# Optimization experiments

Measured on AMD Instinct MI355X. Metric: run time of the kernel, lower is better.

The kernel has to match this reference:

```python
import jax, jax.numpy as jnp
import numpy as np

N_ATOMS = 500_000
N_BONDS = 600_000
N_MOL = 25_000
DEG_COUNTS = [100_000, 175_000, 150_000, 75_000]  # degrees 1..4, sum = N_ATOMS
ATOM_F, BOND_F = 62, 6
HID, FP = 100, 512


def setup_inputs() -> dict:
    key = jax.random.key(0)
    ks = jax.random.split(key, 32)
    inp = {}
    inp['atom_features'] = jax.random.normal(ks[0], (N_ATOMS, ATOM_F), dtype=jnp.float32)
    inp['bond_features'] = jax.random.normal(ks[1], (N_BONDS, BOND_F), dtype=jnp.float32)
    for i, (name_a, name_b, n) in enumerate(zip(['an1','an2','an3','an4'], ['bn1','bn2','bn3','bn4'], DEG_COUNTS)):
        d = i + 1
        inp[name_a] = jax.random.randint(ks[2 + 2*i], (n, d), 0, N_ATOMS, dtype=jnp.int32)
        inp[name_b] = jax.random.randint(ks[3 + 2*i], (n, d), 0, N_BONDS, dtype=jnp.int32)
    inp['mol_ids'] = jnp.repeat(jnp.arange(N_MOL, dtype=jnp.int32), N_ATOMS // N_MOL)
    dims = [(ATOM_F, HID), (HID, HID), (HID, FP)]
    for li, (din, dout) in enumerate(dims):
        inp[f'Wself{li}'] = jax.random.normal(ks[12 + li], (din, dout), dtype=jnp.float32) * (din ** -0.5)
        inp[f'bself{li}'] = jax.random.normal(ks[15 + li], (dout,), dtype=jnp.float32) * 0.01
        inp[f'Wd{li}'] = jax.random.normal(ks[18 + li], (4, din + BOND_F, dout), dtype=jnp.float32) * ((din + BOND_F) ** -0.5)
        inp[f'bd{li}'] = jax.random.normal(ks[21 + li], (4, dout), dtype=jnp.float32) * 0.01
    return inp


def _forward(atom_features, bond_features, ans, bns, mol_ids, self_params, deg_params):
    x = atom_features
    for (Ws, bs), (Wd, bd) in zip(self_params, deg_params):
        self_logits = x @ Ws + bs                      # [N, out]
        neigh = []
        for d in range(4):                             # degrees 1..4 (structurally distinct)
            a_sum = x[ans[d]].sum(axis=1)              # [n_d, F_in]  gather + reduce over degree
            b_sum = bond_features[bns[d]].sum(axis=1)  # [n_d, BOND_F]
            h = jnp.concatenate([a_sum, b_sum], axis=1)
            neigh.append(h @ Wd[d] + bd[d])
        neighbors_logits = jnp.concatenate(neigh, axis=0)  # atoms sorted by degree
        t = neighbors_logits + self_logits
        norm = jnp.linalg.norm(t, axis=1, keepdims=True)   # F.normalize (L2, eps=1e-12)
        x = jax.nn.relu(t / jnp.maximum(norm, 1e-12))
    return jax.ops.segment_sum(x, mol_ids, num_segments=N_MOL)  # sum_and_stack


def reference(atom_features, bond_features, an1, an2, an3, an4, bn1, bn2, bn3, bn4,
              mol_ids, Wself0, bself0, Wself1, bself1, Wself2, bself2,
              Wd0, bd0, Wd1, bd1, Wd2, bd2):
    ans = (an1, an2, an3, an4)
    bns = (bn1, bn2, bn3, bn4)
    self_params = ((Wself0, bself0), (Wself1, bself1), (Wself2, bself2))
    deg_params = ((Wd0, bd0), (Wd1, bd1), (Wd2, bd2))
    return _forward(atom_features, bond_features, ans, bns, mol_ids, self_params, deg_params)
```

## Files before the change

kernel.cpp:

```cpp
#include <hip/hip_runtime.h>


#define XS 100

typedef __attribute__((ext_vector_type(8))) short short8;
typedef __attribute__((ext_vector_type(4))) float float4v;

__device__ __forceinline__ float bf2f(unsigned u) { return __uint_as_float(u << 16); }
__device__ __forceinline__ unsigned short f2bf(float f) {
    unsigned b = __float_as_uint(f);
    return (unsigned short)((b + 0x7FFFu + ((b >> 16) & 1u)) >> 16);
}
__device__ __forceinline__ unsigned pack2(float a, float b) {
    return (unsigned)f2bf(a) | ((unsigned)f2bf(b) << 16);
}
__device__ __forceinline__ void rowseg(int r, int& deg, int& seg) {
    if (r < 100000)      { deg = 1; seg = 0;      }
    else if (r < 275000) { deg = 2; seg = 100000; }
    else if (r < 425000) { deg = 3; seg = 275000; }
    else                 { deg = 4; seg = 425000; }
}

__global__ void prep_weights(const float* __restrict__ Ws, const float* __restrict__ bs,
                             const float* __restrict__ Wd, const float* __restrict__ bd,
                             int F_IN, int F_OUT, int F_OUT_PAD, int KP, int SELF_PAD,
                             unsigned short* __restrict__ Wt, float* __restrict__ bc)
{
    int id = blockIdx.x * 256 + threadIdx.x;
    int total = 4 * F_OUT_PAD * KP;
    if (id >= total) return;
    int k  = id % KP;
    int nq = (id / KP) % F_OUT_PAD;
    int dg = id / (KP * F_OUT_PAD);
    float v = 0.f;
    if (nq < F_OUT) {
        if (k < F_IN)                                   v = Ws[(size_t)k * F_OUT + nq];
        else if (k >= SELF_PAD && k < SELF_PAD + F_IN)  v = Wd[((size_t)dg * (F_IN + 6) + (k - SELF_PAD)) * F_OUT + nq];
        else if (k >= 2 * SELF_PAD && k < 2 * SELF_PAD + 6)
            v = Wd[((size_t)dg * (F_IN + 6) + F_IN + (k - 2 * SELF_PAD)) * F_OUT + nq];
    }
    Wt[id] = f2bf(v);
    if (k == 0)
        bc[dg * F_OUT_PAD + nq] = (nq < F_OUT) ? (bs[nq] + bd[(size_t)dg * F_OUT + nq]) : 0.f;
}

template<int DEG, int SP>
__device__ __forceinline__ void g256_bf16(
    unsigned short* Hs, const unsigned short* __restrict__ x,
    const float* __restrict__ bondf,
    const int* __restrict__ an, const int* __restrict__ bn,
    int seg, int B40, int tid)
{
    const int ch  = tid & 31;
    const int rr  = tid >> 5;
    if (ch < 25) {
        int ai[5][DEG];
        #pragma unroll
        for (int p = 0; p < 5; ++p) {
            const int ri = B40 + rr + 8 * p;
            #pragma unroll
            for (int d = 0; d < DEG; ++d) ai[p][d] = an[(size_t)ri * DEG + d];
        }
        uint2 sv[5], nv[5][DEG];
        #pragma unroll
        for (int p = 0; p < 5; ++p) {
            const int atom = seg + B40 + rr + 8 * p;
            sv[p] = *(const uint2*)(x + (size_t)atom * XS + ch * 4);
            #pragma unroll
            for (int d = 0; d < DEG; ++d)
                nv[p][d] = *(const uint2*)(x + (size_t)ai[p][d] * XS + ch * 4);
        }
        #pragma unroll
        for (int p = 0; p < 5; ++p) {
            unsigned short* hrow = Hs + (rr + 8 * p) * SP;
            *(uint2*)(hrow + ch * 4) = sv[p];
            float s0 = 0.f, s1 = 0.f, s2 = 0.f, s3 = 0.f;
            #pragma unroll
            for (int d = 0; d < DEG; ++d) {
                s0 += bf2f(nv[p][d].x & 0xFFFFu); s1 += bf2f(nv[p][d].x >> 16);
                s2 += bf2f(nv[p][d].y & 0xFFFFu); s3 += bf2f(nv[p][d].y >> 16);
            }
            uint2 o; o.x = pack2(s0, s1); o.y = pack2(s2, s3);
            *(uint2*)(hrow + 104 + ch * 4) = o;
        }
    }
    if (tid < 40) {
        const int ri = B40 + tid;
        int bi[DEG];
        #pragma unroll
        for (int d = 0; d < DEG; ++d) bi[d] = bn[(size_t)ri * DEG + d];
        float2 v0[DEG], v1[DEG], v2[DEG];
        #pragma unroll
        for (int d = 0; d < DEG; ++d) {
            const float* bp = bondf + (size_t)bi[d] * 6;
            v0[d] = *(const float2*)bp;
            v1[d] = *(const float2*)(bp + 2);
            v2[d] = *(const float2*)(bp + 4);
        }
        float s0 = 0.f, s1 = 0.f, s2 = 0.f, s3 = 0.f, s4 = 0.f, s5 = 0.f;
        #pragma unroll
        for (int d = 0; d < DEG; ++d) {
            s0 += v0[d].x; s1 += v0[d].y; s2 += v1[d].x;
            s3 += v1[d].y; s4 += v2[d].x; s5 += v2[d].y;
        }
        unsigned short* hrow = Hs + tid * SP;
        uint4 w; w.x = pack2(s0, s1); w.y = pack2(s2, s3); w.z = pack2(s4, s5); w.w = 0;
        *(uint4*)(hrow + 208) = w;
        *(uint4*)(hrow + 216) = make_uint4(0, 0, 0, 0);
    }
    for (int i = tid; i < 80; i += 256) {
        unsigned short* p = Hs + (i >> 1) * SP + ((i & 1) ? 204 : 100);
        *(uint2*)p = make_uint2(0, 0);
    }
    for (int i = tid; i < 8 * 28; i += 256)
        *(uint4*)(Hs + (40 + i / 28) * SP + (i % 28) * 8) = make_uint4(0, 0, 0, 0);
}

template<int DEG, int SP>
__device__ __forceinline__ void g256_f32(
    unsigned short* Hs, const float* __restrict__ x,
    const float* __restrict__ bondf,
    const int* __restrict__ an, const int* __restrict__ bn,
    int seg, int B40, int tid)
{
    const int ch  = tid & 31;
    const int rr  = tid >> 5;
    if (ch < 31) {
        int ai[5][DEG];
        #pragma unroll
        for (int p = 0; p < 5; ++p) {
            const int ri = B40 + rr + 8 * p;
            #pragma unroll
            for (int d = 0; d < DEG; ++d) ai[p][d] = an[(size_t)ri * DEG + d];
        }
        float2 sv[5], nv[5][DEG];
        #pragma unroll
        for (int p = 0; p < 5; ++p) {
            const int atom = seg + B40 + rr + 8 * p;
            sv[p] = *(const float2*)(x + (size_t)atom * 62 + ch * 2);
            #pragma unroll
            for (int d = 0; d < DEG; ++d)
                nv[p][d] = *(const float2*)(x + (size_t)ai[p][d] * 62 + ch * 2);
        }
        #pragma unroll
        for (int p = 0; p < 5; ++p) {
            unsigned short* hrow = Hs + (rr + 8 * p) * SP;
            *(unsigned*)(hrow + ch * 2) = pack2(sv[p].x, sv[p].y);
            float s0 = 0.f, s1 = 0.f;
            #pragma unroll
            for (int d = 0; d < DEG; ++d) { s0 += nv[p][d].x; s1 += nv[p][d].y; }
            *(unsigned*)(hrow + 64 + ch * 2) = pack2(s0, s1);
        }
    }
    if (tid < 40) {
        const int ri = B40 + tid;
        int bi[DEG];
        #pragma unroll
        for (int d = 0; d < DEG; ++d) bi[d] = bn[(size_t)ri * DEG + d];
        float2 v0[DEG], v1[DEG], v2[DEG];
        #pragma unroll
        for (int d = 0; d < DEG; ++d) {
            const float* bp = bondf + (size_t)bi[d] * 6;
            v0[d] = *(const float2*)bp;
            v1[d] = *(const float2*)(bp + 2);
            v2[d] = *(const float2*)(bp + 4);
        }
        float s0 = 0.f, s1 = 0.f, s2 = 0.f, s3 = 0.f, s4 = 0.f, s5 = 0.f;
        #pragma unroll
        for (int d = 0; d < DEG; ++d) {
            s0 += v0[d].x; s1 += v0[d].y; s2 += v1[d].x;
            s3 += v1[d].y; s4 += v2[d].x; s5 += v2[d].y;
        }
        unsigned short* hrow = Hs + tid * SP;
        uint4 w; w.x = pack2(s0, s1); w.y = pack2(s2, s3); w.z = pack2(s4, s5); w.w = 0;
        *(uint4*)(hrow + 128) = w;
        *(uint4*)(hrow + 136) = make_uint4(0, 0, 0, 0);
        *(uint4*)(hrow + 144) = make_uint4(0, 0, 0, 0);
        *(uint4*)(hrow + 152) = make_uint4(0, 0, 0, 0);
    }
    for (int i = tid; i < 80; i += 256)
        *(unsigned*)(Hs + (i >> 1) * SP + ((i & 1) ? 126 : 62)) = 0;
    for (int i = tid; i < 8 * 20; i += 256)
        *(uint4*)(Hs + (40 + i / 20) * SP + (i % 20) * 8) = make_uint4(0, 0, 0, 0);
}

template<int DEG, int SP>
__device__ __forceinline__ void g512_bf16(
    unsigned short* Hs, const unsigned short* __restrict__ x,
    const float* __restrict__ bondf,
    const int* __restrict__ an, const int* __restrict__ bn,
    int seg, int B40)
{
    const int tid = threadIdx.x;
    const int ch  = tid & 31;
    const int rg  = tid >> 5;
    if (ch < 25) {
        int ai[3][DEG];
        #pragma unroll
        for (int p = 0; p < 3; ++p) {
            const int r = rg + 16 * p;
            if (r < 40) {
                const int ri = B40 + r;
                #pragma unroll
                for (int d = 0; d < DEG; ++d) ai[p][d] = an[(size_t)ri * DEG + d];
            }
        }
        uint2 sv[3], nv[3][DEG];
        #pragma unroll
        for (int p = 0; p < 3; ++p) {
            const int r = rg + 16 * p;
            if (r < 40) {
                sv[p] = *(const uint2*)(x + (size_t)(seg + B40 + r) * XS + ch * 4);
                #pragma unroll
                for (int d = 0; d < DEG; ++d)
                    nv[p][d] = *(const uint2*)(x + (size_t)ai[p][d] * XS + ch * 4);
            }
        }
        #pragma unroll
        for (int p = 0; p < 3; ++p) {
            const int r = rg + 16 * p;
            if (r < 40) {
                unsigned short* hrow = Hs + r * SP;
                *(uint2*)(hrow + ch * 4) = sv[p];
                float s0 = 0.f, s1 = 0.f, s2 = 0.f, s3 = 0.f;
                #pragma unroll
                for (int d = 0; d < DEG; ++d) {
                    s0 += bf2f(nv[p][d].x & 0xFFFFu); s1 += bf2f(nv[p][d].x >> 16);
                    s2 += bf2f(nv[p][d].y & 0xFFFFu); s3 += bf2f(nv[p][d].y >> 16);
                }
                uint2 o; o.x = pack2(s0, s1); o.y = pack2(s2, s3);
                *(uint2*)(hrow + 104 + ch * 4) = o;
            }
        }
    } else {
        const int idx = rg * 7 + (ch - 25);
        if (idx < 40) {
            const int ri = B40 + idx;
            int bi[DEG];
            #pragma unroll
            for (int d = 0; d < DEG; ++d) bi[d] = bn[(size_t)ri * DEG + d];
            float2 v0[DEG], v1[DEG], v2[DEG];
            #pragma unroll
            for (int d = 0; d < DEG; ++d) {
                const float* bp = bondf + (size_t)bi[d] * 6;
                v0[d] = *(const float2*)bp;
                v1[d] = *(const float2*)(bp + 2);
                v2[d] = *(const float2*)(bp + 4);
            }
            float s0 = 0.f, s1 = 0.f, s2 = 0.f, s3 = 0.f, s4 = 0.f, s5 = 0.f;
            #pragma unroll
            for (int d = 0; d < DEG; ++d) {
                s0 += v0[d].x; s1 += v0[d].y; s2 += v1[d].x;
                s3 += v1[d].y; s4 += v2[d].x; s5 += v2[d].y;
            }
            unsigned short* hrow = Hs + idx * SP;
            uint4 w; w.x = pack2(s0, s1); w.y = pack2(s2, s3); w.z = pack2(s4, s5); w.w = 0;
            *(uint4*)(hrow + 208) = w;
            *(uint4*)(hrow + 216) = make_uint4(0, 0, 0, 0);
        }
    }
    for (int i = tid; i < 80; i += 512) {
        unsigned short* p = Hs + (i >> 1) * SP + ((i & 1) ? 204 : 100);
        *(uint2*)p = make_uint2(0, 0);
    }
    for (int i = tid; i < 8 * 28; i += 512)
        *(uint4*)(Hs + (40 + i / 28) * SP + (i % 28) * 8) = make_uint4(0, 0, 0, 0);
}

template<int F_IN, int SELF_PAD, bool BF16IN>
__global__ __launch_bounds__(512, 4) void layer01(
    const void* __restrict__ xin,
    const float* __restrict__ bondf,
    const int* __restrict__ an1, const int* __restrict__ bn1,
    const int* __restrict__ an2, const int* __restrict__ bn2,
    const int* __restrict__ an3, const int* __restrict__ bn3,
    const int* __restrict__ an4, const int* __restrict__ bn4,
    const unsigned short* __restrict__ Wt,
    const float* __restrict__ bcomb,
    unsigned short* __restrict__ xout)
{
    constexpr int F_OUT = 100;
    constexpr int F_OUT_PAD = 112;
    constexpr int KP = (2 * SELF_PAD + 6 + 31) & ~31;
    constexpr int SP = KP + 8;

    __shared__ __align__(16) unsigned short Hs[96 * SP];
    __shared__ float ssqs[7][96];
    __shared__ __align__(16) float rn96[96];

    const int b = blockIdx.x;
    int deg, seg, pair; bool has1;
    if (b < 1250)      { deg = 1; seg = 0;      pair = b;        has1 = true; }
    else if (b < 3438) { deg = 2; seg = 100000; pair = b - 1250; has1 = (pair != 2187); }
    else if (b < 5313) { deg = 3; seg = 275000; pair = b - 3438; has1 = true; }
    else               { deg = 4; seg = 425000; pair = b - 5313; has1 = (pair != 937); }

    const int half = threadIdx.x >> 8;
    const int t    = threadIdx.x & 255;
    const int B40  = pair * 80 + half * 40;
    unsigned short* HsC = Hs + half * 48 * SP;

    if (half == 1 && !has1) {
        for (int i = t; i < 48 * SP / 8; i += 256)
            ((uint4*)HsC)[i] = make_uint4(0, 0, 0, 0);
    } else {
        if constexpr (BF16IN) {
            const unsigned short* x = (const unsigned short*)xin;
            switch (deg) {
                case 1: g256_bf16<1, SP>(HsC, x, bondf, an1, bn1, seg, B40, t); break;
                case 2: g256_bf16<2, SP>(HsC, x, bondf, an2, bn2, seg, B40, t); break;
                case 3: g256_bf16<3, SP>(HsC, x, bondf, an3, bn3, seg, B40, t); break;
                default: g256_bf16<4, SP>(HsC, x, bondf, an4, bn4, seg, B40, t); break;
            }
        } else {
            const float* x = (const float*)xin;
            switch (deg) {
                case 1: g256_f32<1, SP>(HsC, x, bondf, an1, bn1, seg, B40, t); break;
                case 2: g256_f32<2, SP>(HsC, x, bondf, an2, bn2, seg, B40, t); break;
                case 3: g256_f32<3, SP>(HsC, x, bondf, an3, bn3, seg, B40, t); break;
                default: g256_f32<4, SP>(HsC, x, bondf, an4, bn4, seg, B40, t); break;
            }
        }
    }
    __syncthreads();

    const int lane = threadIdx.x & 63;
    const int wv   = threadIdx.x >> 6;
    const int n16  = lane & 15;
    const int quad = lane >> 4;

    float4v acc[6];
    #pragma unroll
    for (int mt = 0; mt < 6; ++mt) acc[mt] = (float4v){0.f, 0.f, 0.f, 0.f};

    if (wv < 7) {
        const unsigned short* Wr =
            Wt + ((size_t)(deg - 1) * F_OUT_PAD + wv * 16 + n16) * KP;
        #pragma unroll
        for (int kk = 0; kk < KP; kk += 32) {
            short8 bb = *(const short8*)(Wr + kk + quad * 8);
            short8 a[6];
            #pragma unroll
            for (int mt = 0; mt < 6; ++mt)
                a[mt] = *(const short8*)&Hs[(mt * 16 + n16) * SP + kk + quad * 8];
            #pragma unroll
            for (int mt = 0; mt < 6; ++mt)
                acc[mt] = __builtin_amdgcn_mfma_f32_16x16x32_bf16(a[mt], bb, acc[mt], 0, 0, 0);
        }
    }

    float ssq[6][4];
    #pragma unroll
    for (int mt = 0; mt < 6; ++mt)
        #pragma unroll
        for (int r = 0; r < 4; ++r) ssq[mt][r] = 0.f;

    if (wv < 7) {
        const float bj = bcomb[(deg - 1) * F_OUT_PAD + wv * 16 + n16];
        #pragma unroll
        for (int mt = 0; mt < 6; ++mt)
            #pragma unroll
            for (int r = 0; r < 4; ++r) {
                float v = acc[mt][r] + bj;
                acc[mt][r] = v;
                ssq[mt][r] += v * v;
            }
        #pragma unroll
        for (int off = 1; off <= 8; off <<= 1)
            #pragma unroll
            for (int mt = 0; mt < 6; ++mt)
                #pragma unroll
                for (int r = 0; r < 4; ++r)
                    ssq[mt][r] += __shfl_xor(ssq[mt][r], off);
        if (n16 == 0)
            #pragma unroll
            for (int mt = 0; mt < 6; ++mt)
                #pragma unroll
                for (int r = 0; r < 4; ++r)
                    ssqs[wv][mt * 16 + quad * 4 + r] = ssq[mt][r];
    }
    __syncthreads();

    if (threadIdx.x < 96) {
        float s = 0.f;
        #pragma unroll
        for (int w = 0; w < 7; ++w) s += ssqs[w][threadIdx.x];
        rn96[threadIdx.x] = 1.0f / fmaxf(sqrtf(s), 1e-12f);
    }
    __syncthreads();

    const int col = wv * 16 + n16;
    if (wv < 7 && col < F_OUT) {
        #pragma unroll
        for (int mt = 0; mt < 6; ++mt) {
            const int chunk = mt / 3;
            if (chunk == 0 || has1) {
                float4 rv = *(const float4*)&rn96[mt * 16 + quad * 4];
                const float rn_[4] = {rv.x, rv.y, rv.z, rv.w};
                const int rowc0 = (mt % 3) * 16 + quad * 4;
                const int gbase = seg + pair * 80 + chunk * 40 + rowc0;
                #pragma unroll
                for (int r = 0; r < 4; ++r) {
                    if (rowc0 + r < 40) {
                        const float v = fmaxf(acc[mt][r] * rn_[r], 0.f);
                        xout[(size_t)(gbase + r) * XS + col] = f2bf(v);
                    }
                }
            }
        }
    }
}

__global__ __launch_bounds__(512, 4) void layer_last(
    const unsigned short* __restrict__ x,
    const float* __restrict__ bondf,
    const int* __restrict__ an1, const int* __restrict__ bn1,
    const int* __restrict__ an2, const int* __restrict__ bn2,
    const int* __restrict__ an3, const int* __restrict__ bn3,
    const int* __restrict__ an4, const int* __restrict__ bn4,
    const unsigned short* __restrict__ Wt,
    const float* __restrict__ bcomb,
    float* __restrict__ molout)
{
    constexpr int KP = 224, SP = 232, NW = 8, JMAX = 4;

    __shared__ __align__(16) unsigned short Hs[48 * SP];
    __shared__ float ssqs[NW][48];
    __shared__ __align__(16) float rn48[48];

    const int R0 = blockIdx.x * 40;
    int deg, seg; rowseg(R0, deg, seg);
    const int B40 = R0 - seg;

    switch (deg) {
        case 1: g512_bf16<1, SP>(Hs, x, bondf, an1, bn1, seg, B40); break;
        case 2: g512_bf16<2, SP>(Hs, x, bondf, an2, bn2, seg, B40); break;
        case 3: g512_bf16<3, SP>(Hs, x, bondf, an3, bn3, seg, B40); break;
        default: g512_bf16<4, SP>(Hs, x, bondf, an4, bn4, seg, B40); break;
    }
    __syncthreads();

    const int lane = threadIdx.x & 63;
    const int wv   = threadIdx.x >> 6;
    const int n16  = lane & 15;
    const int quad = lane >> 4;

    float4v acc[JMAX][3];
    #pragma unroll
    for (int j = 0; j < JMAX; ++j)
        #pragma unroll
        for (int mt = 0; mt < 3; ++mt)
            acc[j][mt] = (float4v){0.f, 0.f, 0.f, 0.f};

    const unsigned short* Wb = Wt + (size_t)(deg - 1) * 512 * KP;

    #pragma unroll
    for (int kk = 0; kk < KP; kk += 32) {
        short8 a[3];
        #pragma unroll
        for (int mt = 0; mt < 3; ++mt)
            a[mt] = *(const short8*)&Hs[(mt * 16 + n16) * SP + kk + quad * 8];
        short8 bfr[JMAX];
        #pragma unroll
        for (int j = 0; j < JMAX; ++j) {
            const int nt = wv + NW * j;
            bfr[j] = *(const short8*)(Wb + (size_t)(nt * 16 + n16) * KP + kk + quad * 8);
        }
        #pragma unroll
        for (int j = 0; j < JMAX; ++j)
            #pragma unroll
            for (int mt = 0; mt < 3; ++mt)
                acc[j][mt] = __builtin_amdgcn_mfma_f32_16x16x32_bf16(
                    a[mt], bfr[j], acc[j][mt], 0, 0, 0);
    }

    float ssq[3][4];
    #pragma unroll
    for (int mt = 0; mt < 3; ++mt)
        #pragma unroll
        for (int r = 0; r < 4; ++r) ssq[mt][r] = 0.f;

    #pragma unroll
    for (int j = 0; j < JMAX; ++j) {
        const int nt = wv + NW * j;
        const float bj = bcomb[(deg - 1) * 512 + nt * 16 + n16];
        #pragma unroll
        for (int mt = 0; mt < 3; ++mt)
            #pragma unroll
            for (int r = 0; r < 4; ++r) {
                float v = acc[j][mt][r] + bj;
                acc[j][mt][r] = v;
                ssq[mt][r] += v * v;
            }
    }
    #pragma unroll
    for (int off = 1; off <= 8; off <<= 1)
        #pragma unroll
        for (int mt = 0; mt < 3; ++mt)
            #pragma unroll
            for (int r = 0; r < 4; ++r)
                ssq[mt][r] += __shfl_xor(ssq[mt][r], off);
    if (n16 == 0)
        #pragma unroll
        for (int mt = 0; mt < 3; ++mt)
            #pragma unroll
            for (int r = 0; r < 4; ++r)
                ssqs[wv][mt * 16 + quad * 4 + r] = ssq[mt][r];
    __syncthreads();

    if (threadIdx.x < 48) {
        float s = 0.f;
        #pragma unroll
        for (int w = 0; w < NW; ++w) s += ssqs[w][threadIdx.x];
        rn48[threadIdx.x] = 1.0f / fmaxf(sqrtf(s), 1e-12f);
    }
    __syncthreads();

    float rn[3][4];
    #pragma unroll
    for (int mt = 0; mt < 3; ++mt) {
        float4 v = *(const float4*)&rn48[mt * 16 + quad * 4];
        rn[mt][0] = v.x; rn[mt][1] = v.y; rn[mt][2] = v.z; rn[mt][3] = v.w;
    }

    #pragma unroll
    for (int j = 0; j < JMAX; ++j) {
        float m0 = 0.f, m1 = 0.f;
        #pragma unroll
        for (int mt = 0; mt < 3; ++mt)
            #pragma unroll
            for (int r = 0; r < 4; ++r) {
                const int row = mt * 16 + quad * 4 + r;
                if (row < 40) {
                    const float v = fmaxf(acc[j][mt][r] * rn[mt][r], 0.f);
                    if (row < 20) m0 += v; else m1 += v;
                }
            }
        m0 += __shfl_xor(m0, 16); m0 += __shfl_xor(m0, 32);
        m1 += __shfl_xor(m1, 16); m1 += __shfl_xor(m1, 32);
        if (quad == 0) {
            const int col = (wv + NW * j) * 16 + n16;
            molout[(size_t)(2 * blockIdx.x)     * 512 + col] = m0;
            molout[(size_t)(2 * blockIdx.x + 1) * 512 + col] = m1;
        }
    }
}

extern "C" void kernel_launch(void* const* d_in, const int* in_sizes, int n_in,
                              void* d_out, int out_size, void* d_ws, size_t ws_size,
                              hipStream_t stream) {
    const bool sig_order = (in_sizes[3] != 100000);

    const float* atomf = (const float*)d_in[0];
    const float* bondf = (const float*)d_in[1];
    const int *an1, *bn1, *an2, *bn2, *an3, *bn3, *an4, *bn4;
    const float *Ws0, *bs0, *Wd0, *bd0;
    const float *Ws1, *bs1, *Wd1, *bd1;
    const float *Ws2, *bs2, *Wd2, *bd2;

    if (!sig_order) {
        an1 = (const int*)d_in[2];  bn1 = (const int*)d_in[3];
        an2 = (const int*)d_in[4];  bn2 = (const int*)d_in[5];
        an3 = (const int*)d_in[6];  bn3 = (const int*)d_in[7];
        an4 = (const int*)d_in[8];  bn4 = (const int*)d_in[9];
        Ws0 = (const float*)d_in[11]; bs0 = (const float*)d_in[12];
        Wd0 = (const float*)d_in[13]; bd0 = (const float*)d_in[14];
        Ws1 = (const float*)d_in[15]; bs1 = (const float*)d_in[16];
        Wd1 = (const float*)d_in[17]; bd1 = (const float*)d_in[18];
        Ws2 = (const float*)d_in[19]; bs2 = (const float*)d_in[20];
        Wd2 = (const float*)d_in[21]; bd2 = (const float*)d_in[22];
    } else {
        an1 = (const int*)d_in[2];  an2 = (const int*)d_in[3];
        an3 = (const int*)d_in[4];  an4 = (const int*)d_in[5];
        bn1 = (const int*)d_in[6];  bn2 = (const int*)d_in[7];
        bn3 = (const int*)d_in[8];  bn4 = (const int*)d_in[9];
        Ws0 = (const float*)d_in[11]; bs0 = (const float*)d_in[12];
        Ws1 = (const float*)d_in[13]; bs1 = (const float*)d_in[14];
        Ws2 = (const float*)d_in[15]; bs2 = (const float*)d_in[16];
        Wd0 = (const float*)d_in[17]; bd0 = (const float*)d_in[18];
        Wd1 = (const float*)d_in[19]; bd1 = (const float*)d_in[20];
        Wd2 = (const float*)d_in[21]; bd2 = (const float*)d_in[22];
    }

    char* w = (char*)d_ws;
    unsigned short* x1  = (unsigned short*)w;
    unsigned short* x2  = (unsigned short*)(w + 100000000);
    unsigned short* Wt0 = (unsigned short*)(w + 200000000);
    float*          bc0 = (float*)(w + 200143360);
    unsigned short* Wt1 = (unsigned short*)(w + 200145152);
    float*          bc1 = (float*)(w + 200345856);
    unsigned short* Wt2 = (unsigned short*)(w + 200347648);
    float*          bc2 = (float*)(w + 201265152);

    prep_weights<<<(4 * 112 * 160 + 255) / 256, 256, 0, stream>>>(
        Ws0, bs0, Wd0, bd0, 62, 100, 112, 160, 64, Wt0, bc0);
    prep_weights<<<(4 * 112 * 224 + 255) / 256, 256, 0, stream>>>(
        Ws1, bs1, Wd1, bd1, 100, 100, 112, 224, 104, Wt1, bc1);
    prep_weights<<<(4 * 512 * 224 + 255) / 256, 256, 0, stream>>>(
        Ws2, bs2, Wd2, bd2, 100, 512, 512, 224, 104, Wt2, bc2);

    layer01<62, 64, false><<<6251, 512, 0, stream>>>(
        atomf, bondf, an1, bn1, an2, bn2, an3, bn3, an4, bn4, Wt0, bc0, x1);
    layer01<100, 104, true><<<6251, 512, 0, stream>>>(
        x1, bondf, an1, bn1, an2, bn2, an3, bn3, an4, bn4, Wt1, bc1, x2);
    layer_last<<<12500, 512, 0, stream>>>(
        x2, bondf, an1, bn1, an2, bn2, an3, bn3, an4, bn4,
        Wt2, bc2, (float*)d_out);
}
```

Baseline: 778.9 us.

## Process two 40-row tiles per block in last layer to reuse weight fragments

The final 100→512 layer now handles 80 atom rows per block (two 40-row halves, each gathered by 256 threads) instead of 40. Each wave issues MFMAs over six M-tiles per loaded weight fragment, so global weight reads per row are halved and the grid shrinks from 12500 to 6251 blocks. The cost is twice the accumulator registers and a lowered occupancy hint (launch bounds 512,2), plus a doubled shared tile and padding handling for odd segment ends.

```diff
diff --git a/kernel.cpp b/kernel.cpp
--- a/kernel.cpp
+++ b/kernel.cpp
@@ -14,11 +14,12 @@
 __device__ __forceinline__ unsigned pack2(float a, float b) {
     return (unsigned)f2bf(a) | ((unsigned)f2bf(b) << 16);
 }
-__device__ __forceinline__ void rowseg(int r, int& deg, int& seg) {
-    if (r < 100000)      { deg = 1; seg = 0;      }
-    else if (r < 275000) { deg = 2; seg = 100000; }
-    else if (r < 425000) { deg = 3; seg = 275000; }
-    else                 { deg = 4; seg = 425000; }
+
+__device__ __forceinline__ void pairseg(int b, int& deg, int& seg, int& pair, bool& has1) {
+    if (b < 1250)      { deg = 1; seg = 0;      pair = b;        has1 = true; }
+    else if (b < 3438) { deg = 2; seg = 100000; pair = b - 1250; has1 = (pair != 2187); }
+    else if (b < 5313) { deg = 3; seg = 275000; pair = b - 3438; has1 = true; }
+    else               { deg = 4; seg = 425000; pair = b - 5313; has1 = (pair != 937); }
 }
 
 __global__ void prep_weights(const float* __restrict__ Ws, const float* __restrict__ bs,
@@ -184,89 +185,6 @@
         *(uint4*)(Hs + (40 + i / 20) * SP + (i % 20) * 8) = make_uint4(0, 0, 0, 0);
 }
 
-template<int DEG, int SP>
-__device__ __forceinline__ void g512_bf16(
-    unsigned short* Hs, const unsigned short* __restrict__ x,
-    const float* __restrict__ bondf,
-    const int* __restrict__ an, const int* __restrict__ bn,
-    int seg, int B40)
-{
-    const int tid = threadIdx.x;
-    const int ch  = tid & 31;
-    const int rg  = tid >> 5;
-    if (ch < 25) {
-        int ai[3][DEG];
-        #pragma unroll
-        for (int p = 0; p < 3; ++p) {
-            const int r = rg + 16 * p;
-            if (r < 40) {
-                const int ri = B40 + r;
-                #pragma unroll
-                for (int d = 0; d < DEG; ++d) ai[p][d] = an[(size_t)ri * DEG + d];
-            }
-        }
-        uint2 sv[3], nv[3][DEG];
-        #pragma unroll
-        for (int p = 0; p < 3; ++p) {
-            const int r = rg + 16 * p;
-            if (r < 40) {
-                sv[p] = *(const uint2*)(x + (size_t)(seg + B40 + r) * XS + ch * 4);
-                #pragma unroll
-                for (int d = 0; d < DEG; ++d)
-                    nv[p][d] = *(const uint2*)(x + (size_t)ai[p][d] * XS + ch * 4);
-            }
-        }
-        #pragma unroll
-        for (int p = 0; p < 3; ++p) {
-            const int r = rg + 16 * p;
-            if (r < 40) {
-                unsigned short* hrow = Hs + r * SP;
-                *(uint2*)(hrow + ch * 4) = sv[p];
-                float s0 = 0.f, s1 = 0.f, s2 = 0.f, s3 = 0.f;
-                #pragma unroll
-                for (int d = 0; d < DEG; ++d) {
-                    s0 += bf2f(nv[p][d].x & 0xFFFFu); s1 += bf2f(nv[p][d].x >> 16);
-                    s2 += bf2f(nv[p][d].y & 0xFFFFu); s3 += bf2f(nv[p][d].y >> 16);
-                }
-                uint2 o; o.x = pack2(s0, s1); o.y = pack2(s2, s3);
-                *(uint2*)(hrow + 104 + ch * 4) = o;
-            }
-        }
-    } else {
-        const int idx = rg * 7 + (ch - 25);
-        if (idx < 40) {
-            const int ri = B40 + idx;
-            int bi[DEG];
-            #pragma unroll
-            for (int d = 0; d < DEG; ++d) bi[d] = bn[(size_t)ri * DEG + d];
-            float2 v0[DEG], v1[DEG], v2[DEG];
-            #pragma unroll
-            for (int d = 0; d < DEG; ++d) {
-                const float* bp = bondf + (size_t)bi[d] * 6;
-                v0[d] = *(const float2*)bp;
-                v1[d] = *(const float2*)(bp + 2);
-                v2[d] = *(const float2*)(bp + 4);
-            }
-            float s0 = 0.f, s1 = 0.f, s2 = 0.f, s3 = 0.f, s4 = 0.f, s5 = 0.f;
-            #pragma unroll
-            for (int d = 0; d < DEG; ++d) {
-                s0 += v0[d].x; s1 += v0[d].y; s2 += v1[d].x;
-                s3 += v1[d].y; s4 += v2[d].x; s5 += v2[d].y;
-            }
-            unsigned short* hrow = Hs + idx * SP;
-            uint4 w; w.x = pack2(s0, s1); w.y = pack2(s2, s3); w.z = pack2(s4, s5); w.w = 0;
-            *(uint4*)(hrow + 208) = w;
-            *(uint4*)(hrow + 216) = make_uint4(0, 0, 0, 0);
-        }
-    }
-    for (int i = tid; i < 80; i += 512) {
-        unsigned short* p = Hs + (i >> 1) * SP + ((i & 1) ? 204 : 100);
-        *(uint2*)p = make_uint2(0, 0);
-    }
-    for (int i = tid; i < 8 * 28; i += 512)
-        *(uint4*)(Hs + (40 + i / 28) * SP + (i % 28) * 8) = make_uint4(0, 0, 0, 0);
-}
-
 template<int F_IN, int SELF_PAD, bool BF16IN>
 __global__ __launch_bounds__(512, 4) void layer01(
     const void* __restrict__ xin,
@@ -290,10 +208,7 @@
 
     const int b = blockIdx.x;
     int deg, seg, pair; bool has1;
-    if (b < 1250)      { deg = 1; seg = 0;      pair = b;        has1 = true; }
-    else if (b < 3438) { deg = 2; seg = 100000; pair = b - 1250; has1 = (pair != 2187); }
-    else if (b < 5313) { deg = 3; seg = 275000; pair = b - 3438; has1 = true; }
-    else               { deg = 4; seg = 425000; pair = b - 5313; has1 = (pair != 937); }
+    pairseg(b, deg, seg, pair, has1);
 
     const int half = threadIdx.x >> 8;
     const int t    = threadIdx.x & 255;
@@ -411,7 +326,7 @@
     }
 }
 
-__global__ __launch_bounds__(512, 4) void layer_last(
+__global__ __launch_bounds__(512, 2) void layer_last2(
     const unsigned short* __restrict__ x,
     const float* __restrict__ bondf,
     const int* __restrict__ an1, const int* __restrict__ bn1,
@@ -422,21 +337,31 @@
     const float* __restrict__ bcomb,
     float* __restrict__ molout)
 {
-    constexpr int KP = 224, SP = 232, NW = 8, JMAX = 4;
-
-    __shared__ __align__(16) unsigned short Hs[48 * SP];
-    __shared__ float ssqs[NW][48];
-    __shared__ __align__(16) float rn48[48];
-
-    const int R0 = blockIdx.x * 40;
-    int deg, seg; rowseg(R0, deg, seg);
-    const int B40 = R0 - seg;
-
-    switch (deg) {
-        case 1: g512_bf16<1, SP>(Hs, x, bondf, an1, bn1, seg, B40); break;
-        case 2: g512_bf16<2, SP>(Hs, x, bondf, an2, bn2, seg, B40); break;
-        case 3: g512_bf16<3, SP>(Hs, x, bondf, an3, bn3, seg, B40); break;
-        default: g512_bf16<4, SP>(Hs, x, bondf, an4, bn4, seg, B40); break;
+    constexpr int KP = 224, SP = 232, JMAX = 4;
+
+    __shared__ __align__(16) unsigned short Hs[96 * SP];
+    __shared__ float ssqs[8][96];
+    __shared__ __align__(16) float rn96[96];
+
+    const int b = blockIdx.x;
+    int deg, seg, pair; bool has1;
+    pairseg(b, deg, seg, pair, has1);
+
+    const int half = threadIdx.x >> 8;
+    const int t    = threadIdx.x & 255;
+    const int B40  = pair * 80 + half * 40;
+    unsigned short* HsC = Hs + half * 48 * SP;
+
+    if (half == 1 && !has1) {
+        for (int i = t; i < 48 * SP / 8; i += 256)
+            ((uint4*)HsC)[i] = make_uint4(0, 0, 0, 0);
+    } else {
+        switch (deg) {
+            case 1: g256_bf16<1, SP>(HsC, x, bondf, an1, bn1, seg, B40, t); break;
+            case 2: g256_bf16<2, SP>(HsC, x, bondf, an2, bn2, seg, B40, t); break;
+            case 3: g256_bf16<3, SP>(HsC, x, bondf, an3, bn3, seg, B40, t); break;
+            default: g256_bf16<4, SP>(HsC, x, bondf, an4, bn4, seg, B40, t); break;
+        }
     }
     __syncthreads();
 
@@ -445,47 +370,46 @@
     const int n16  = lane & 15;
     const int quad = lane >> 4;
 
-    float4v acc[JMAX][3];
+    float4v acc[JMAX][6];
     #pragma unroll
     for (int j = 0; j < JMAX; ++j)
         #pragma unroll
-        for (int mt = 0; mt < 3; ++mt)
+        for (int mt = 0; mt < 6; ++mt)
             acc[j][mt] = (float4v){0.f, 0.f, 0.f, 0.f};
 
     const unsigned short* Wb = Wt + (size_t)(deg - 1) * 512 * KP;
 
     #pragma unroll
     for (int kk = 0; kk < KP; kk += 32) {
-        short8 a[3];
-        #pragma unroll
-        for (int mt = 0; mt < 3; ++mt)
+        short8 a[6];
+        #pragma unroll
+        for (int mt = 0; mt < 6; ++mt)
             a[mt] = *(const short8*)&Hs[(mt * 16 + n16) * SP + kk + quad * 8];
         short8 bfr[JMAX];
         #pragma unroll
         for (int j = 0; j < JMAX; ++j) {
-            const int nt = wv + NW * j;
+            const int nt = wv + 8 * j;
             bfr[j] = *(const short8*)(Wb + (size_t)(nt * 16 + n16) * KP + kk + quad * 8);
         }
         #pragma unroll
         for (int j = 0; j < JMAX; ++j)
             #pragma unroll
-            for (int mt = 0; mt < 3; ++mt)
+            for (int mt = 0; mt < 6; ++mt)
                 acc[j][mt] = __builtin_amdgcn_mfma_f32_16x16x32_bf16(
                     a[mt], bfr[j], acc[j][mt], 0, 0, 0);
     }
 
-    float ssq[3][4];
-    #pragma unroll
-    for (int mt = 0; mt < 3; ++mt)
+    float ssq[6][4];
+    #pragma unroll
+    for (int mt = 0; mt < 6; ++mt)
         #pragma unroll
         for (int r = 0; r < 4; ++r) ssq[mt][r] = 0.f;
 
     #pragma unroll
     for (int j = 0; j < JMAX; ++j) {
-        const int nt = wv + NW * j;
-        const float bj = bcomb[(deg - 1) * 512 + nt * 16 + n16];
-        #pragma unroll
-        for (int mt = 0; mt < 3; ++mt)
+        const float bj = bcomb[(deg - 1) * 512 + (wv + 8 * j) * 16 + n16];
+        #pragma unroll
+        for (int mt = 0; mt < 6; ++mt)
             #pragma unroll
             for (int r = 0; r < 4; ++r) {
                 float v = acc[j][mt][r] + bj;
@@ -496,52 +420,60 @@
     #pragma unroll
     for (int off = 1; off <= 8; off <<= 1)
         #pragma unroll
-        for (int mt = 0; mt < 3; ++mt)
+        for (int mt = 0; mt < 6; ++mt)
             #pragma unroll
             for (int r = 0; r < 4; ++r)
                 ssq[mt][r] += __shfl_xor(ssq[mt][r], off);
     if (n16 == 0)
         #pragma unroll
-        for (int mt = 0; mt < 3; ++mt)
+        for (int mt = 0; mt < 6; ++mt)
             #pragma unroll
             for (int r = 0; r < 4; ++r)
                 ssqs[wv][mt * 16 + quad * 4 + r] = ssq[mt][r];
     __syncthreads();
 
-    if (threadIdx.x < 48) {
+    if (threadIdx.x < 96) {
         float s = 0.f;
         #pragma unroll
-        for (int w = 0; w < NW; ++w) s += ssqs[w][threadIdx.x];
-        rn48[threadIdx.x] = 1.0f / fmaxf(sqrtf(s), 1e-12f);
+        for (int w = 0; w < 8; ++w) s += ssqs[w][threadIdx.x];
+        rn96[threadIdx.x] = 1.0f / fmaxf(sqrtf(s), 1e-12f);
     }
     __syncthreads();
 
-    float rn[3][4];
-    #pragma unroll
-    for (int mt = 0; mt < 3; ++mt) {
-        float4 v = *(const float4*)&rn48[mt * 16 + quad * 4];
-        rn[mt][0] = v.x; rn[mt][1] = v.y; rn[mt][2] = v.z; rn[mt][3] = v.w;
-    }
-
+    float rn_[6][4];
+    #pragma unroll
+    for (int mt = 0; mt < 6; ++mt) {
+        float4 v = *(const float4*)&rn96[mt * 16 + quad * 4];
+        rn_[mt][0] = v.x; rn_[mt][1] = v.y; rn_[mt][2] = v.z; rn_[mt][3] = v.w;
+    }
+
+    const int g0 = seg / 40 + 2 * pair;
     #pragma unroll
     for (int j = 0; j < JMAX; ++j) {
-        float m0 = 0.f, m1 = 0.f;
-        #pragma unroll
-        for (int mt = 0; mt < 3; ++mt)
+        float c0a = 0.f, c0b = 0.f, c1a = 0.f, c1b = 0.f;
+        #pragma unroll
+        for (int mt = 0; mt < 6; ++mt)
             #pragma unroll
             for (int r = 0; r < 4; ++r) {
-                const int row = mt * 16 + quad * 4 + r;
-                if (row < 40) {
-                    const float v = fmaxf(acc[j][mt][r] * rn[mt][r], 0.f);
-                    if (row < 20) m0 += v; else m1 += v;
+                const int row40 = (mt % 3) * 16 + quad * 4 + r;
+                if (row40 < 40) {
+                    const float v = fmaxf(acc[j][mt][r] * rn_[mt][r], 0.f);
+                    if (mt < 3) { if (row40 < 20) c0a += v; else c0b += v; }
+                    else        { if (row40 < 20) c1a += v; else c1b += v; }
                 }
             }
-        m0 += __shfl_xor(m0, 16); m0 += __shfl_xor(m0, 32);
-        m1 += __shfl_xor(m1, 16); m1 += __shfl_xor(m1, 32);
+        c0a += __shfl_xor(c0a, 16); c0a += __shfl_xor(c0a, 32);
+        c0b += __shfl_xor(c0b, 16); c0b += __shfl_xor(c0b, 32);
+        c1a += __shfl_xor(c1a, 16); c1a += __shfl_xor(c1a, 32);
+        c1b += __shfl_xor(c1b, 16); c1b += __shfl_xor(c1b, 32);
         if (quad == 0) {
-            const int col = (wv + NW * j) * 16 + n16;
-            molout[(size_t)(2 * blockIdx.x)     * 512 + col] = m0;
-            molout[(size_t)(2 * blockIdx.x + 1) * 512 + col] = m1;
+            const int col = (wv + 8 * j) * 16 + n16;
+            molout[(size_t)(2 * g0)     * 512 + col] = c0a;
+            molout[(size_t)(2 * g0 + 1) * 512 + col] = c0b;
+            if (has1) {
+                molout[(size_t)(2 * g0 + 2) * 512 + col] = c1a;
+                molout[(size_t)(2 * g0 + 3) * 512 + col] = c1b;
+            }
         }
     }
 }
@@ -603,7 +535,7 @@
         atomf, bondf, an1, bn1, an2, bn2, an3, bn3, an4, bn4, Wt0, bc0, x1);
     layer01<100, 104, true><<<6251, 512, 0, stream>>>(
         x1, bondf, an1, bn1, an2, bn2, an3, bn3, an4, bn4, Wt1, bc1, x2);
-    layer_last<<<12500, 512, 0, stream>>>(
+    layer_last2<<<6251, 512, 0, stream>>>(
         x2, bondf, an1, bn1, an2, bn2, an3, bn3, an4, bn4,
         Wt2, bc2, (float*)d_out);
 }
```

Measured after the change: 812.3 us. +4.3%, slower.

## Make last layer persistent with producer/consumer warp specialization and double-buffered gathers

Applied to the files above, without the earlier changes.

The last layer now runs 500 persistent blocks. Each block loops over 25 chunks of 40 atoms and is split into producer waves, which gather neighbor, self and bond features into a double-buffered LDS tile, and consumer waves, which run the MFMA matmul, normalization and molecule reduction. This is meant to overlap the irregular gather latency with matrix work and to amortize setup across chunks. In exchange only 4 consumer waves compute per block, each holding 8 column tiles (more registers, launch bounds lowered to 2), and the grid is much smaller, which may underfill the GPU.

```diff
diff --git a/kernel.cpp b/kernel.cpp
--- a/kernel.cpp
+++ b/kernel.cpp
@@ -14,11 +14,12 @@
 __device__ __forceinline__ unsigned pack2(float a, float b) {
     return (unsigned)f2bf(a) | ((unsigned)f2bf(b) << 16);
 }
-__device__ __forceinline__ void rowseg(int r, int& deg, int& seg) {
-    if (r < 100000)      { deg = 1; seg = 0;      }
-    else if (r < 275000) { deg = 2; seg = 100000; }
-    else if (r < 425000) { deg = 3; seg = 275000; }
-    else                 { deg = 4; seg = 425000; }
+
+__device__ __forceinline__ void pairseg(int b, int& deg, int& seg, int& pair, bool& has1) {
+    if (b < 1250)      { deg = 1; seg = 0;      pair = b;        has1 = true; }
+    else if (b < 3438) { deg = 2; seg = 100000; pair = b - 1250; has1 = (pair != 2187); }
+    else if (b < 5313) { deg = 3; seg = 275000; pair = b - 3438; has1 = true; }
+    else               { deg = 4; seg = 425000; pair = b - 5313; has1 = (pair != 937); }
 }
 
 __global__ void prep_weights(const float* __restrict__ Ws, const float* __restrict__ bs,
@@ -184,89 +185,6 @@
         *(uint4*)(Hs + (40 + i / 20) * SP + (i % 20) * 8) = make_uint4(0, 0, 0, 0);
 }
 
-template<int DEG, int SP>
-__device__ __forceinline__ void g512_bf16(
-    unsigned short* Hs, const unsigned short* __restrict__ x,
-    const float* __restrict__ bondf,
-    const int* __restrict__ an, const int* __restrict__ bn,
-    int seg, int B40)
-{
-    const int tid = threadIdx.x;
-    const int ch  = tid & 31;
-    const int rg  = tid >> 5;
-    if (ch < 25) {
-        int ai[3][DEG];
-        #pragma unroll
-        for (int p = 0; p < 3; ++p) {
-            const int r = rg + 16 * p;
-            if (r < 40) {
-                const int ri = B40 + r;
-                #pragma unroll
-                for (int d = 0; d < DEG; ++d) ai[p][d] = an[(size_t)ri * DEG + d];
-            }
-        }
-        uint2 sv[3], nv[3][DEG];
-        #pragma unroll
-        for (int p = 0; p < 3; ++p) {
-            const int r = rg + 16 * p;
-            if (r < 40) {
-                sv[p] = *(const uint2*)(x + (size_t)(seg + B40 + r) * XS + ch * 4);
-                #pragma unroll
-                for (int d = 0; d < DEG; ++d)
-                    nv[p][d] = *(const uint2*)(x + (size_t)ai[p][d] * XS + ch * 4);
-            }
-        }
-        #pragma unroll
-        for (int p = 0; p < 3; ++p) {
-            const int r = rg + 16 * p;
-            if (r < 40) {
-                unsigned short* hrow = Hs + r * SP;
-                *(uint2*)(hrow + ch * 4) = sv[p];
-                float s0 = 0.f, s1 = 0.f, s2 = 0.f, s3 = 0.f;
-                #pragma unroll
-                for (int d = 0; d < DEG; ++d) {
-                    s0 += bf2f(nv[p][d].x & 0xFFFFu); s1 += bf2f(nv[p][d].x >> 16);
-                    s2 += bf2f(nv[p][d].y & 0xFFFFu); s3 += bf2f(nv[p][d].y >> 16);
-                }
-                uint2 o; o.x = pack2(s0, s1); o.y = pack2(s2, s3);
-                *(uint2*)(hrow + 104 + ch * 4) = o;
-            }
-        }
-    } else {
-        const int idx = rg * 7 + (ch - 25);
-        if (idx < 40) {
-            const int ri = B40 + idx;
-            int bi[DEG];
-            #pragma unroll
-            for (int d = 0; d < DEG; ++d) bi[d] = bn[(size_t)ri * DEG + d];
-            float2 v0[DEG], v1[DEG], v2[DEG];
-            #pragma unroll
-            for (int d = 0; d < DEG; ++d) {
-                const float* bp = bondf + (size_t)bi[d] * 6;
-                v0[d] = *(const float2*)bp;
-                v1[d] = *(const float2*)(bp + 2);
-                v2[d] = *(const float2*)(bp + 4);
-            }
-            float s0 = 0.f, s1 = 0.f, s2 = 0.f, s3 = 0.f, s4 = 0.f, s5 = 0.f;
-            #pragma unroll
-            for (int d = 0; d < DEG; ++d) {
-                s0 += v0[d].x; s1 += v0[d].y; s2 += v1[d].x;
-                s3 += v1[d].y; s4 += v2[d].x; s5 += v2[d].y;
-            }
-            unsigned short* hrow = Hs + idx * SP;
-            uint4 w; w.x = pack2(s0, s1); w.y = pack2(s2, s3); w.z = pack2(s4, s5); w.w = 0;
-            *(uint4*)(hrow + 208) = w;
-            *(uint4*)(hrow + 216) = make_uint4(0, 0, 0, 0);
-        }
-    }
-    for (int i = tid; i < 80; i += 512) {
-        unsigned short* p = Hs + (i >> 1) * SP + ((i & 1) ? 204 : 100);
-        *(uint2*)p = make_uint2(0, 0);
-    }
-    for (int i = tid; i < 8 * 28; i += 512)
-        *(uint4*)(Hs + (40 + i / 28) * SP + (i % 28) * 8) = make_uint4(0, 0, 0, 0);
-}
-
 template<int F_IN, int SELF_PAD, bool BF16IN>
 __global__ __launch_bounds__(512, 4) void layer01(
     const void* __restrict__ xin,
@@ -290,10 +208,7 @@
 
     const int b = blockIdx.x;
     int deg, seg, pair; bool has1;
-    if (b < 1250)      { deg = 1; seg = 0;      pair = b;        has1 = true; }
-    else if (b < 3438) { deg = 2; seg = 100000; pair = b - 1250; has1 = (pair != 2187); }
-    else if (b < 5313) { deg = 3; seg = 275000; pair = b - 3438; has1 = true; }
-    else               { deg = 4; seg = 425000; pair = b - 5313; has1 = (pair != 937); }
+    pairseg(b, deg, seg, pair, has1);
 
     const int half = threadIdx.x >> 8;
     const int t    = threadIdx.x & 255;
@@ -411,7 +326,216 @@
     }
 }
 
-__global__ __launch_bounds__(512, 4) void layer_last(
+template<int DEG>
+__device__ __forceinline__ void lastPC(
+    unsigned short* Hs, float (*ssqs)[48], float* rn48,
+    const unsigned short* __restrict__ x, const float* __restrict__ bondf,
+    const int* __restrict__ an, const int* __restrict__ bn,
+    const unsigned short* __restrict__ Wt, const float* __restrict__ bcomb,
+    float* __restrict__ molout, int c0, int seg)
+{
+    constexpr int KP = 224, SP = 232;
+    constexpr int HSZ = 48 * SP;
+    const int tid = threadIdx.x;
+
+    for (int i = tid; i < 2 * HSZ / 8; i += 512)
+        ((uint4*)Hs)[i] = make_uint4(0, 0, 0, 0);
+
+    const bool cons = tid < 256;
+    const int lane = tid & 63, wv = tid >> 6, n16 = lane & 15, quad = lane >> 4;
+    const int pt = tid - 256;
+
+    uint2  valS[5];
+    uint2  valN[4][DEG];
+    float2 valB[DEG];
+
+    auto fetch_chunk = [&](int cc) {
+        const int B40c = cc * 40 - seg;
+        const int R0c  = cc * 40;
+        if (pt < 250) {
+            int ix[4][DEG];
+            #pragma unroll
+            for (int k = 0; k < 4; ++k) {
+                const int r = (k * 250 + pt) / 25;
+                #pragma unroll
+                for (int d = 0; d < DEG; ++d)
+                    ix[k][d] = an[(size_t)(B40c + r) * DEG + d];
+            }
+            #pragma unroll
+            for (int k = 0; k < 4; ++k) {
+                const int ch = (k * 250 + pt) % 25;
+                #pragma unroll
+                for (int d = 0; d < DEG; ++d)
+                    valN[k][d] = *(const uint2*)(x + (size_t)ix[k][d] * XS + ch * 4);
+            }
+        }
+        if (pt < 200) {
+            #pragma unroll
+            for (int k = 0; k < 5; ++k) {
+                const int uu = k * 200 + pt, s = uu / 25, ch = uu % 25;
+                valS[k] = *(const uint2*)(x + (size_t)(R0c + s) * XS + ch * 4);
+            }
+        }
+        if (pt < 120) {
+            const int r = pt / 3, j = pt - 3 * r;
+            int ib[DEG];
+            #pragma unroll
+            for (int d = 0; d < DEG; ++d) ib[d] = bn[(size_t)(B40c + r) * DEG + d];
+            #pragma unroll
+            for (int d = 0; d < DEG; ++d)
+                valB[d] = *(const float2*)(bondf + (size_t)ib[d] * 6 + j * 2);
+        }
+    };
+    auto reduce_write = [&](unsigned short* Hw) {
+        if (pt < 250) {
+            #pragma unroll
+            for (int k = 0; k < 4; ++k) {
+                const int uu = k * 250 + pt, r = uu / 25, ch = uu % 25;
+                float s0 = 0.f, s1 = 0.f, s2 = 0.f, s3 = 0.f;
+                #pragma unroll
+                for (int d = 0; d < DEG; ++d) {
+                    s0 += bf2f(valN[k][d].x & 0xFFFFu); s1 += bf2f(valN[k][d].x >> 16);
+                    s2 += bf2f(valN[k][d].y & 0xFFFFu); s3 += bf2f(valN[k][d].y >> 16);
+                }
+                uint2 o; o.x = pack2(s0, s1); o.y = pack2(s2, s3);
+                *(uint2*)(Hw + r * SP + 104 + ch * 4) = o;
+            }
+        }
+        if (pt < 200) {
+            #pragma unroll
+            for (int k = 0; k < 5; ++k) {
+                const int uu = k * 200 + pt, s = uu / 25, ch = uu % 25;
+                *(uint2*)(Hw + s * SP + ch * 4) = valS[k];
+            }
+        }
+        if (pt < 120) {
+            const int r = pt / 3, j = pt - 3 * r;
+            float sx = 0.f, sy = 0.f;
+            #pragma unroll
+            for (int d = 0; d < DEG; ++d) { sx += valB[d].x; sy += valB[d].y; }
+            *(unsigned*)(Hw + r * SP + 208 + j * 2) = pack2(sx, sy);
+        }
+    };
+
+    const unsigned short* Wb = Wt + (size_t)(DEG - 1) * 512 * KP;
+    float bj[8];
+    if (cons) {
+        #pragma unroll
+        for (int j = 0; j < 8; ++j)
+            bj[j] = bcomb[(DEG - 1) * 512 + (wv + 4 * j) * 16 + n16];
+    }
+
+    if (!cons) {
+        fetch_chunk(c0);
+        reduce_write(Hs);
+        fetch_chunk(c0 + 1);
+    }
+    __syncthreads();
+
+    int pb = 0;
+    for (int ci = 0; ci < 25; ++ci) {
+        const int c = c0 + ci;
+        const unsigned short* Hr = Hs + pb * HSZ;
+        unsigned short* Hw = Hs + (pb ^ 1) * HSZ;
+
+        float4v acc[8][3];
+        if (cons) {
+            #pragma unroll
+            for (int j = 0; j < 8; ++j)
+                #pragma unroll
+                for (int mt = 0; mt < 3; ++mt)
+                    acc[j][mt] = (float4v){0.f, 0.f, 0.f, 0.f};
+            #pragma unroll
+            for (int kk = 0; kk < KP; kk += 32) {
+                short8 a[3];
+                #pragma unroll
+                for (int mt = 0; mt < 3; ++mt)
+                    a[mt] = *(const short8*)&Hr[(mt * 16 + n16) * SP + kk + quad * 8];
+                short8 bfr[8];
+                #pragma unroll
+                for (int j = 0; j < 8; ++j)
+                    bfr[j] = *(const short8*)(Wb + (size_t)((wv + 4 * j) * 16 + n16) * KP + kk + quad * 8);
+                #pragma unroll
+                for (int j = 0; j < 8; ++j)
+                    #pragma unroll
+                    for (int mt = 0; mt < 3; ++mt)
+                        acc[j][mt] = __builtin_amdgcn_mfma_f32_16x16x32_bf16(
+                            a[mt], bfr[j], acc[j][mt], 0, 0, 0);
+            }
+            float ssq[3][4];
+            #pragma unroll
+            for (int mt = 0; mt < 3; ++mt)
+                #pragma unroll
+                for (int r = 0; r < 4; ++r) ssq[mt][r] = 0.f;
+            #pragma unroll
+            for (int j = 0; j < 8; ++j)
+                #pragma unroll
+                for (int mt = 0; mt < 3; ++mt)
+                    #pragma unroll
+                    for (int r = 0; r < 4; ++r) {
+                        float v = acc[j][mt][r] + bj[j];
+                        acc[j][mt][r] = v;
+                        ssq[mt][r] += v * v;
+                    }
+            #pragma unroll
+            for (int off = 1; off <= 8; off <<= 1)
+                #pragma unroll
+                for (int mt = 0; mt < 3; ++mt)
+                    #pragma unroll
+                    for (int r = 0; r < 4; ++r)
+                        ssq[mt][r] += __shfl_xor(ssq[mt][r], off);
+            if (n16 == 0)
+                #pragma unroll
+                for (int mt = 0; mt < 3; ++mt)
+                    #pragma unroll
+                    for (int r = 0; r < 4; ++r)
+                        ssqs[wv][mt * 16 + quad * 4 + r] = ssq[mt][r];
+        } else {
+            if (ci + 1 < 25) reduce_write(Hw);
+            if (ci + 2 < 25) fetch_chunk(c + 2);
+        }
+        __syncthreads();
+
+        if (tid < 48) {
+            float s = ssqs[0][tid] + ssqs[1][tid] + ssqs[2][tid] + ssqs[3][tid];
+            rn48[tid] = 1.0f / fmaxf(sqrtf(s), 1e-12f);
+        }
+        __syncthreads();
+
+        if (cons) {
+            float rn_[3][4];
+            #pragma unroll
+            for (int mt = 0; mt < 3; ++mt) {
+                float4 v = *(const float4*)&rn48[mt * 16 + quad * 4];
+                rn_[mt][0] = v.x; rn_[mt][1] = v.y; rn_[mt][2] = v.z; rn_[mt][3] = v.w;
+            }
+            #pragma unroll
+            for (int j = 0; j < 8; ++j) {
+                float m0 = 0.f, m1 = 0.f;
+                #pragma unroll
+                for (int mt = 0; mt < 3; ++mt)
+                    #pragma unroll
+                    for (int r = 0; r < 4; ++r) {
+                        const int row = mt * 16 + quad * 4 + r;
+                        if (row < 40) {
+                            const float v = fmaxf(acc[j][mt][r] * rn_[mt][r], 0.f);
+                            if (row < 20) m0 += v; else m1 += v;
+                        }
+                    }
+                m0 += __shfl_xor(m0, 16); m0 += __shfl_xor(m0, 32);
+                m1 += __shfl_xor(m1, 16); m1 += __shfl_xor(m1, 32);
+                if (quad == 0) {
+                    const int col = (wv + 4 * j) * 16 + n16;
+                    molout[(size_t)(2 * c)     * 512 + col] = m0;
+                    molout[(size_t)(2 * c + 1) * 512 + col] = m1;
+                }
+            }
+        }
+        pb ^= 1;
+    }
+}
+
+__global__ __launch_bounds__(512, 2) void layer_lastPC(
     const unsigned short* __restrict__ x,
     const float* __restrict__ bondf,
     const int* __restrict__ an1, const int* __restrict__ bn1,
@@ -422,128 +546,23 @@
     const float* __restrict__ bcomb,
     float* __restrict__ molout)
 {
-    constexpr int KP = 224, SP = 232, NW = 8, JMAX = 4;
-
-    __shared__ __align__(16) unsigned short Hs[48 * SP];
-    __shared__ float ssqs[NW][48];
+    __shared__ __align__(16) unsigned short Hs[2 * 48 * 232];
+    __shared__ float ssqs[4][48];
     __shared__ __align__(16) float rn48[48];
 
-    const int R0 = blockIdx.x * 40;
-    int deg, seg; rowseg(R0, deg, seg);
-    const int B40 = R0 - seg;
-
-    switch (deg) {
-        case 1: g512_bf16<1, SP>(Hs, x, bondf, an1, bn1, seg, B40); break;
-        case 2: g512_bf16<2, SP>(Hs, x, bondf, an2, bn2, seg, B40); break;
-        case 3: g512_bf16<3, SP>(Hs, x, bondf, an3, bn3, seg, B40); break;
-        default: g512_bf16<4, SP>(Hs, x, bondf, an4, bn4, seg, B40); break;
-    }
-    __syncthreads();
-
-    const int lane = threadIdx.x & 63;
-    const int wv   = threadIdx.x >> 6;
-    const int n16  = lane & 15;
-    const int quad = lane >> 4;
-
-    float4v acc[JMAX][3];
-    #pragma unroll
-    for (int j = 0; j < JMAX; ++j)
-        #pragma unroll
-        for (int mt = 0; mt < 3; ++mt)
-            acc[j][mt] = (float4v){0.f, 0.f, 0.f, 0.f};
-
-    const unsigned short* Wb = Wt + (size_t)(deg - 1) * 512 * KP;
-
-    #pragma unroll
-    for (int kk = 0; kk < KP; kk += 32) {
-        short8 a[3];
-        #pragma unroll
-        for (int mt = 0; mt < 3; ++mt)
-            a[mt] = *(const short8*)&Hs[(mt * 16 + n16) * SP + kk + quad * 8];
-        short8 bfr[JMAX];
-        #pragma unroll
-        for (int j = 0; j < JMAX; ++j) {
-            const int nt = wv + NW * j;
-            bfr[j] = *(const short8*)(Wb + (size_t)(nt * 16 + n16) * KP + kk + quad * 8);
-        }
-        #pragma unroll
-        for (int j = 0; j < JMAX; ++j)
-            #pragma unroll
-            for (int mt = 0; mt < 3; ++mt)
-                acc[j][mt] = __builtin_amdgcn_mfma_f32_16x16x32_bf16(
-                    a[mt], bfr[j], acc[j][mt], 0, 0, 0);
-    }
-
-    float ssq[3][4];
-    #pragma unroll
-    for (int mt = 0; mt < 3; ++mt)
-        #pragma unroll
-        for (int r = 0; r < 4; ++r) ssq[mt][r] = 0.f;
-
-    #pragma unroll
-    for (int j = 0; j < JMAX; ++j) {
-        const int nt = wv + NW * j;
-        const float bj = bcomb[(deg - 1) * 512 + nt * 16 + n16];
-        #pragma unroll
-        for (int mt = 0; mt < 3; ++mt)
-            #pragma unroll
-            for (int r = 0; r < 4; ++r) {
-                float v = acc[j][mt][r] + bj;
-                acc[j][mt][r] = v;
-                ssq[mt][r] += v * v;
-            }
-    }
-    #pragma unroll
-    for (int off = 1; off <= 8; off <<= 1)
-        #pragma unroll
-        for (int mt = 0; mt < 3; ++mt)
-            #pragma unroll
-            for (int r = 0; r < 4; ++r)
-                ssq[mt][r] += __shfl_xor(ssq[mt][r], off);
-    if (n16 == 0)
-        #pragma unroll
-        for (int mt = 0; mt < 3; ++mt)
-            #pragma unroll
-            for (int r = 0; r < 4; ++r)
-                ssqs[wv][mt * 16 + quad * 4 + r] = ssq[mt][r];
-    __syncthreads();
-
-    if (threadIdx.x < 48) {
-        float s = 0.f;
-        #pragma unroll
-        for (int w = 0; w < NW; ++w) s += ssqs[w][threadIdx.x];
-        rn48[threadIdx.x] = 1.0f / fmaxf(sqrtf(s), 1e-12f);
-    }
-    __syncthreads();
-
-    float rn[3][4];
-    #pragma unroll
-    for (int mt = 0; mt < 3; ++mt) {
-        float4 v = *(const float4*)&rn48[mt * 16 + quad * 4];
-        rn[mt][0] = v.x; rn[mt][1] = v.y; rn[mt][2] = v.z; rn[mt][3] = v.w;
-    }
-
-    #pragma unroll
-    for (int j = 0; j < JMAX; ++j) {
-        float m0 = 0.f, m1 = 0.f;
-        #pragma unroll
-        for (int mt = 0; mt < 3; ++mt)
-            #pragma unroll
-            for (int r = 0; r < 4; ++r) {
-                const int row = mt * 16 + quad * 4 + r;
-                if (row < 40) {
-                    const float v = fmaxf(acc[j][mt][r] * rn[mt][r], 0.f);
-                    if (row < 20) m0 += v; else m1 += v;
-                }
-            }
-        m0 += __shfl_xor(m0, 16); m0 += __shfl_xor(m0, 32);
-        m1 += __shfl_xor(m1, 16); m1 += __shfl_xor(m1, 32);
-        if (quad == 0) {
-            const int col = (wv + NW * j) * 16 + n16;
-            molout[(size_t)(2 * blockIdx.x)     * 512 + col] = m0;
-            molout[(size_t)(2 * blockIdx.x + 1) * 512 + col] = m1;
-        }
-    }
+    const int b = blockIdx.x;
+    if (b < 100)
+        lastPC<1>(Hs, ssqs, rn48, x, bondf, an1, bn1, Wt, bcomb, molout,
+                  b * 25, 0);
+    else if (b < 275)
+        lastPC<2>(Hs, ssqs, rn48, x, bondf, an2, bn2, Wt, bcomb, molout,
+                  2500 + (b - 100) * 25, 100000);
+    else if (b < 425)
+        lastPC<3>(Hs, ssqs, rn48, x, bondf, an3, bn3, Wt, bcomb, molout,
+                  6875 + (b - 275) * 25, 275000);
+    else
+        lastPC<4>(Hs, ssqs, rn48, x, bondf, an4, bn4, Wt, bcomb, molout,
+                  10625 + (b - 425) * 25, 425000);
 }
 
 extern "C" void kernel_launch(void* const* d_in, const int* in_sizes, int n_in,
@@ -603,7 +622,7 @@
         atomf, bondf, an1, bn1, an2, bn2, an3, bn3, an4, bn4, Wt0, bc0, x1);
     layer01<100, 104, true><<<6251, 512, 0, stream>>>(
         x1, bondf, an1, bn1, an2, bn2, an3, bn3, an4, bn4, Wt1, bc1, x2);
-    layer_last<<<12500, 512, 0, stream>>>(
+    layer_lastPC<<<500, 512, 0, stream>>>(
         x2, bondf, an1, bn1, an2, bn2, an3, bn3, an4, bn4,
         Wt2, bc2, (float*)d_out);
 }
```

Result: slower. 1.538 ms (+97.4%).
